# Optimization experiments

Hardware: AMD Instinct MI355X
Metric: run time of the kernel (lower is better)

## Reference

```python
import jax, jax.numpy as jnp
import numpy as np

D_MODEL = 1024
NUM_HEADS = 16
D_K = D_MODEL // NUM_HEADS
FFN_SIZE = 4096
EPS = 1e-6


def _layer_norm(x, gamma, beta):
    mu = jnp.mean(x, axis=-1, keepdims=True)
    var = jnp.var(x, axis=-1, keepdims=True)
    return (x - mu) / jnp.sqrt(var + EPS) * gamma + beta


def setup_inputs() -> dict:
    key = jax.random.key(0)
    ks = jax.random.split(key, 12)
    B, S = 2, 2048
    s_attn = 1.0 / np.sqrt(D_MODEL)
    s_ffn1 = 1.0 / np.sqrt(D_MODEL)
    s_ffn2 = 1.0 / np.sqrt(FFN_SIZE)
    return {
        "x": jax.random.normal(ks[0], (B, S, D_MODEL), dtype=jnp.float32),
        "W_q": jax.random.normal(ks[1], (D_MODEL, D_MODEL), dtype=jnp.float32) * s_attn,
        "W_k": jax.random.normal(ks[2], (D_MODEL, D_MODEL), dtype=jnp.float32) * s_attn,
        "W_v": jax.random.normal(ks[3], (D_MODEL, D_MODEL), dtype=jnp.float32) * s_attn,
        "W_o": jax.random.normal(ks[4], (D_MODEL, D_MODEL), dtype=jnp.float32) * s_attn,
        "b_o": jnp.zeros((D_MODEL,), dtype=jnp.float32),
        "W1": jax.random.normal(ks[5], (D_MODEL, FFN_SIZE), dtype=jnp.float32) * s_ffn1,
        "b1": jnp.zeros((FFN_SIZE,), dtype=jnp.float32),
        "W2": jax.random.normal(ks[6], (FFN_SIZE, D_MODEL), dtype=jnp.float32) * s_ffn2,
        "b2": jnp.zeros((D_MODEL,), dtype=jnp.float32),
        "ln1_g": jnp.ones((D_MODEL,), dtype=jnp.float32),
        "ln1_b": jnp.zeros((D_MODEL,), dtype=jnp.float32),
        "ln2_g": jnp.ones((D_MODEL,), dtype=jnp.float32),
        "ln2_b": jnp.zeros((D_MODEL,), dtype=jnp.float32),
    }


def reference(x, W_q, W_k, W_v, W_o, b_o, W1, b1, W2, b2,
              ln1_g, ln1_b, ln2_g, ln2_b):
    B, S, _ = x.shape

    # --- self-attention sublayer (pre-norm residual) ---
    h = _layer_norm(x, ln1_g, ln1_b)
    q = (h @ W_q).reshape(B, S, NUM_HEADS, D_K).transpose(0, 2, 1, 3)  # [B,H,S,Dk]
    k = (h @ W_k).reshape(B, S, NUM_HEADS, D_K).transpose(0, 2, 1, 3)
    v = (h @ W_v).reshape(B, S, NUM_HEADS, D_K).transpose(0, 2, 1, 3)
    scores = jnp.einsum("bhqd,bhkd->bhqk", q, k) / jnp.sqrt(jnp.float32(D_K))
    attn = jax.nn.softmax(scores, axis=-1)
    ctx = jnp.einsum("bhqk,bhkd->bhqd", attn, v)
    ctx = ctx.transpose(0, 2, 1, 3).reshape(B, S, D_MODEL)
    x = x + (ctx @ W_o + b_o)

    # --- FFN sublayer (pre-norm residual) ---
    h2 = _layer_norm(x, ln2_g, ln2_b)
    f = jax.nn.relu(h2 @ W1 + b1) @ W2 + b2
    return x + f
```

## Files before the change

### kernel.cpp

```cpp
#include <hip/hip_runtime.h>
#include <cstdint>
#include <cstddef>


typedef __attribute__((ext_vector_type(8))) __bf16 bf16x8;
typedef __attribute__((ext_vector_type(4))) __bf16 bf16x4;
typedef __attribute__((ext_vector_type(4))) float f32x4;

__device__ __forceinline__ void async16(const void* g, void* l) {
  __builtin_amdgcn_global_load_lds(
      (__attribute__((address_space(1))) void*)g,
      (__attribute__((address_space(3))) void*)l, 16, 0, 0);
}

__device__ __forceinline__ f32x4 mfma16(bf16x8 a, bf16x8 b, f32x4 c) {
  return __builtin_amdgcn_mfma_f32_16x16x32_bf16(a, b, c, 0, 0, 0);
}

template <int N>
__device__ __forceinline__ void wait_vmcnt() {
  if constexpr (N == 0) {
    asm volatile("s_waitcnt vmcnt(0)" ::: "memory");
  } else if constexpr (N == 3) {
    asm volatile("s_waitcnt vmcnt(3)" ::: "memory");
  } else {
    asm volatile("s_waitcnt vmcnt(4)" ::: "memory");
  }
}
__device__ __forceinline__ void barrier_raw() {
  asm volatile("s_barrier" ::: "memory");
}

__global__ __launch_bounds__(256) void transpose_all(
    const float* __restrict__ Wq, const float* __restrict__ Wk,
    const float* __restrict__ Wv, const float* __restrict__ Wo,
    const float* __restrict__ W1, const float* __restrict__ W2,
    __bf16* __restrict__ WqkvT, __bf16* __restrict__ WoT,
    __bf16* __restrict__ W1T, __bf16* __restrict__ W2T) {
  const int id = blockIdx.x;
  const float* in;
  __bf16* out;
  int ld_in, ld_out, c0, r0;
  if (id < 1024) {
    const int which = id >> 8, tl = id & 255;
    c0 = (tl & 15) * 64;
    r0 = (tl >> 4) * 64;
    ld_in = 1024;
    ld_out = 1024;
    if (which == 0) { in = Wq; out = WqkvT; }
    else if (which == 1) { in = Wk; out = WqkvT + 1048576; }
    else if (which == 2) { in = Wv; out = WqkvT + 2097152; }
    else { in = Wo; out = WoT; }
  } else if (id < 2048) {
    const int tl = id - 1024;
    c0 = (tl & 63) * 64;
    r0 = (tl >> 6) * 64;
    in = W1; out = W1T; ld_in = 4096; ld_out = 1024;
  } else {
    const int tl = id - 2048;
    c0 = (tl & 15) * 64;
    r0 = (tl >> 4) * 64;
    in = W2; out = W2T; ld_in = 1024; ld_out = 4096;
  }
  __shared__ __bf16 tile[64][65];
  const int tx = threadIdx.x & 63, ty = threadIdx.x >> 6;
#pragma unroll
  for (int i = 0; i < 16; i++) {
    int r = ty + i * 4;
    tile[r][tx] = (__bf16)in[(size_t)(r0 + r) * ld_in + c0 + tx];
  }
  __syncthreads();
#pragma unroll
  for (int i = 0; i < 16; i++) {
    int r = ty + i * 4;
    out[(size_t)(c0 + r) * ld_out + r0 + tx] = tile[tx][r];
  }
}

__global__ __launch_bounds__(256) void transpose_bf16(
    const unsigned short* __restrict__ in, unsigned short* __restrict__ out,
    int ld_in, int ld_out) {
  __shared__ unsigned short tile[64][65];
  const int c0 = blockIdx.x * 64, r0 = blockIdx.y * 64;
  const int tx = threadIdx.x & 63, ty = threadIdx.x >> 6;
#pragma unroll
  for (int i = 0; i < 16; i++) {
    int r = ty + i * 4;
    tile[r][tx] = in[(size_t)(r0 + r) * ld_in + c0 + tx];
  }
  __syncthreads();
#pragma unroll
  for (int i = 0; i < 16; i++) {
    int r = ty + i * 4;
    out[(size_t)(c0 + r) * ld_out + r0 + tx] = tile[tx][r];
  }
}

__global__ __launch_bounds__(256) void ln_kernel(
    const float* __restrict__ xin, const float* __restrict__ g,
    const float* __restrict__ bt, __bf16* __restrict__ out) {
  const int tok = blockIdx.x * 4 + (threadIdx.x >> 6);
  const int lane = threadIdx.x & 63;
  const int base0 = lane * 8, base1 = 512 + lane * 8;
  const float* xr = xin + (size_t)tok * 1024;
  float v[16];
  float4 a0 = *(const float4*)(xr + base0);
  float4 a1 = *(const float4*)(xr + base0 + 4);
  float4 a2 = *(const float4*)(xr + base1);
  float4 a3 = *(const float4*)(xr + base1 + 4);
  v[0] = a0.x; v[1] = a0.y; v[2] = a0.z; v[3] = a0.w;
  v[4] = a1.x; v[5] = a1.y; v[6] = a1.z; v[7] = a1.w;
  v[8] = a2.x; v[9] = a2.y; v[10] = a2.z; v[11] = a2.w;
  v[12] = a3.x; v[13] = a3.y; v[14] = a3.z; v[15] = a3.w;
  float s = 0.f, s2 = 0.f;
#pragma unroll
  for (int i = 0; i < 16; i++) { s += v[i]; s2 += v[i] * v[i]; }
#pragma unroll
  for (int m = 1; m < 64; m <<= 1) {
    s += __shfl_xor(s, m);
    s2 += __shfl_xor(s2, m);
  }
  const float mean = s * (1.f / 1024.f);
  const float var = s2 * (1.f / 1024.f) - mean * mean;
  const float rstd = rsqrtf(var + 1e-6f);
  float4 g0 = *(const float4*)(g + base0), g1 = *(const float4*)(g + base0 + 4);
  float4 g2 = *(const float4*)(g + base1), g3 = *(const float4*)(g + base1 + 4);
  float4 b0 = *(const float4*)(bt + base0), b1v = *(const float4*)(bt + base0 + 4);
  float4 b2v = *(const float4*)(bt + base1), b3 = *(const float4*)(bt + base1 + 4);
  float gg[16] = {g0.x, g0.y, g0.z, g0.w, g1.x, g1.y, g1.z, g1.w,
                  g2.x, g2.y, g2.z, g2.w, g3.x, g3.y, g3.z, g3.w};
  float bb[16] = {b0.x, b0.y, b0.z, b0.w, b1v.x, b1v.y, b1v.z, b1v.w,
                  b2v.x, b2v.y, b2v.z, b2v.w, b3.x, b3.y, b3.z, b3.w};
  bf16x8 o0, o1;
#pragma unroll
  for (int j = 0; j < 8; j++) {
    o0[j] = (__bf16)((v[j] - mean) * rstd * gg[j] + bb[j]);
    o1[j] = (__bf16)((v[8 + j] - mean) * rstd * gg[8 + j] + bb[8 + j]);
  }
  __bf16* op = out + (size_t)tok * 1024;
  *(bf16x8*)(op + base0) = o0;
  *(bf16x8*)(op + base1) = o1;
}

template <int EPI, int TM, int SPLITS = 1>
__global__ __launch_bounds__(256) void gemm_bt(
    const __bf16* __restrict__ A, int lda, const __bf16* __restrict__ BT,
    int ldb, void* __restrict__ C, int ldc, int Kb,
    const float* __restrict__ bias, const float* __restrict__ res, int ldres) {
  const int t = threadIdx.x;
  const int m0 = blockIdx.x * TM, n0 = blockIdx.y * 128;
  const int kz = (SPLITS > 1) ? blockIdx.z : 0;
  __shared__ __align__(16) __bf16 As[3][TM * 32];
  __shared__ __align__(16) __bf16 Bs[3][128 * 32];
  const int lane = t & 63, w = t >> 6;
  const int quad = lane >> 4, l15 = lane & 15;
  const int wm = w >> 1, wn = w & 1;
  constexpr int MF = TM / 32;
  constexpr int LOADS = TM / 64 + 2;

  f32x4 acc[MF][4] = {};

  const int swc = ((t & 3) ^ ((t >> 3) & 3)) * 8;
  const __bf16* ga = A + (size_t)(m0 + (t >> 2)) * lda + swc + (size_t)kz * Kb;
  const __bf16* gb = BT + (size_t)(n0 + (t >> 2)) * ldb + swc + (size_t)kz * Kb;
  const size_t a64 = (size_t)64 * lda, b64 = (size_t)64 * ldb;

  auto stage = [&](int buf) {
#pragma unroll
    for (int i = 0; i < TM / 64; i++)
      async16(ga + i * a64, As[buf] + t * 8 + i * 2048);
    async16(gb, Bs[buf] + t * 8);
    async16(gb + b64, Bs[buf] + t * 8 + 2048);
    ga += 32;
    gb += 32;
  };
  const int ce = (quad ^ ((l15 >> 1) & 3)) * 8;
  auto compute = [&](int buf) {
    bf16x8 af[MF], bfr[4];
#pragma unroll
    for (int i = 0; i < MF; i++)
      af[i] = *(const bf16x8*)&As[buf][(wm * (TM / 2) + i * 16 + l15) * 32 + ce];
#pragma unroll
    for (int i = 0; i < 4; i++)
      bfr[i] = *(const bf16x8*)&Bs[buf][(wn * 64 + i * 16 + l15) * 32 + ce];
#pragma unroll
    for (int mi = 0; mi < MF; mi++)
#pragma unroll
      for (int ni = 0; ni < 4; ni++)
        acc[mi][ni] = mfma16(af[mi], bfr[ni], acc[mi][ni]);
  };

  const int iters = Kb / 32;
  stage(0);
  stage(1);
  int cur = 0, stg = 2;
  for (int it = 0; it < iters - 1; ++it) {
    wait_vmcnt<LOADS>();
    barrier_raw();
    if (it + 2 < iters) stage(stg);
    compute(cur);
    cur = (cur == 2) ? 0 : cur + 1;
    stg = (stg == 2) ? 0 : stg + 1;
  }
  wait_vmcnt<0>();
  barrier_raw();
  compute(cur);

  float biasv[4];
  if constexpr (EPI != 0) {
#pragma unroll
    for (int ni = 0; ni < 4; ni++)
      biasv[ni] = bias[n0 + wn * 64 + ni * 16 + l15];
  }
  __bf16* Cb = (__bf16*)C;
  if constexpr (SPLITS > 1)
    Cb += (size_t)kz * gridDim.x * TM * ldc;
#pragma unroll
  for (int mi = 0; mi < MF; mi++)
#pragma unroll
    for (int ni = 0; ni < 4; ni++)
#pragma unroll
      for (int r = 0; r < 4; r++) {
        const int row = m0 + wm * (TM / 2) + mi * 16 + quad * 4 + r;
        const int col = n0 + wn * 64 + ni * 16 + l15;
        float v = acc[mi][ni][r];
        if constexpr (EPI == 0) {
          Cb[(size_t)row * ldc + col] = (__bf16)v;
        } else if constexpr (EPI == 1) {
          v += biasv[ni] + res[(size_t)row * ldres + col];
          ((float*)C)[(size_t)row * ldc + col] = v;
        } else {
          v += biasv[ni];
          ((__bf16*)C)[(size_t)row * ldc + col] = (__bf16)fmaxf(v, 0.f);
        }
      }
}

__global__ __launch_bounds__(256) void reduce_split(
    const __bf16* __restrict__ P, const float* __restrict__ bias,
    const float* __restrict__ res, float* __restrict__ out) {
  const int row = blockIdx.x, c = threadIdx.x * 4;
  const size_t i = (size_t)row * 1024 + c;
  bf16x4 p0 = *(const bf16x4*)(P + i);
  bf16x4 p1 = *(const bf16x4*)(P + 4194304 + i);
  float4 r = *(const float4*)(res + i);
  float4 bv = *(const float4*)(bias + c);
  float4 o;
  o.x = (float)p0[0] + (float)p1[0] + r.x + bv.x;
  o.y = (float)p0[1] + (float)p1[1] + r.y + bv.y;
  o.z = (float)p0[2] + (float)p1[2] + r.z + bv.z;
  o.w = (float)p0[3] + (float)p1[3] + r.w + bv.w;
  *(float4*)(out + i) = o;
}

__global__ __launch_bounds__(256, 4) void attn_kernel(
    const __bf16* __restrict__ QKV, const __bf16* __restrict__ VT,
    __bf16* __restrict__ ctx) {
  const int qt = blockIdx.x, bh = blockIdx.y;
  const int b = bh >> 4, h = bh & 15;
  const int t = threadIdx.x, w = t >> 6, lane = t & 63;
  const int quad = lane >> 4, l15 = lane & 15;
  const int tok0 = b * 2048;
  const int q0w = tok0 + qt * 64 + w * 16;

  __shared__ __align__(16) __bf16 Ks[128 * 64];
  __shared__ __align__(16) __bf16 VTs[64 * 128];

  const float qs = 0.18033688011112042f;
  bf16x8 qf[2];
#pragma unroll
  for (int kb = 0; kb < 2; kb++) {
    const __bf16* src =
        QKV + (size_t)(q0w + l15) * 3072 + h * 64 + kb * 32 + quad * 8;
    bf16x8 r = *(const bf16x8*)src;
#pragma unroll
    for (int j = 0; j < 8; j++) r[j] = (__bf16)((float)r[j] * qs);
    qf[kb] = r;
  }

  f32x4 lacc = {};
  f32x4 O[4] = {};

  const int krow = t >> 3;
  const int kcg = (((t & 7) ^ (krow & 7)) * 8);
  const int vrow = t >> 4;
  const int vcg = (((2 * (t & 15)) ^ ((vrow & 7) * 2)) * 4);
  const int sub = 4 * (quad & 1);
  const int qh = quad >> 1;

  for (int kt = 0; kt < 16; ++kt) {
    const int ktok = tok0 + kt * 128;
#pragma unroll
    for (int j = 0; j < 4; j++) {
      const __bf16* gp =
          QKV + (size_t)(ktok + krow + j * 32) * 3072 + 1024 + h * 64 + kcg;
      async16(gp, Ks + t * 8 + j * 2048);
    }
#pragma unroll
    for (int j = 0; j < 4; j++) {
      const __bf16* gp =
          VT + (size_t)(h * 64 + vrow + j * 16) * 4096 + ktok + vcg;
      async16(gp, VTs + t * 8 + j * 2048);
    }
    __syncthreads();

    f32x4 sT[8];
#pragma unroll
    for (int kt8 = 0; kt8 < 8; kt8++) {
      f32x4 a = {};
#pragma unroll
      for (int kb = 0; kb < 2; kb++) {
        bf16x8 kf = *(const bf16x8*)&Ks[(kt8 * 16 + l15) * 64 +
                                        (((kb * 4 + quad) ^ (l15 & 7)) * 8)];
        a = mfma16(kf, qf[kb], a);
      }
      sT[kt8] = a;
    }

    bf16x8 pf[4];
#pragma unroll
    for (int kb = 0; kb < 4; kb++)
#pragma unroll
      for (int hf = 0; hf < 2; hf++)
#pragma unroll
        for (int r = 0; r < 4; r++) {
          const float p = __builtin_amdgcn_exp2f(sT[2 * kb + hf][r]);
          lacc[r] += p;
          pf[kb][hf * 4 + r] = (__bf16)p;
        }

#pragma unroll
    for (int kb = 0; kb < 4; kb++) {
      const int g0 = (((4 * kb + qh) ^ (l15 & 7)) * 8) + sub;
      const int g1 = (((4 * kb + 2 + qh) ^ (l15 & 7)) * 8) + sub;
#pragma unroll
      for (int nd = 0; nd < 4; nd++) {
        const int base = (nd * 16 + l15) * 128;
        bf16x4 a0 = *(const bf16x4*)&VTs[base + g0];
        bf16x4 a1 = *(const bf16x4*)&VTs[base + g1];
        bf16x8 vf;
        vf[0] = a0[0]; vf[1] = a0[1]; vf[2] = a0[2]; vf[3] = a0[3];
        vf[4] = a1[0]; vf[5] = a1[1]; vf[6] = a1[2]; vf[7] = a1[3];
        O[nd] = mfma16(pf[kb], vf, O[nd]);
      }
    }
    __syncthreads();
  }

  float lsum = lacc[0] + lacc[1] + lacc[2] + lacc[3];
  lsum += __shfl_xor(lsum, 16);
  lsum += __shfl_xor(lsum, 32);
  float rl[4];
#pragma unroll
  for (int r = 0; r < 4; r++) rl[r] = 1.0f / __shfl(lsum, quad * 4 + r);
#pragma unroll
  for (int nd = 0; nd < 4; nd++)
#pragma unroll
    for (int r = 0; r < 4; r++) {
      const int tokq = q0w + quad * 4 + r;
      const int col = h * 64 + nd * 16 + l15;
      ctx[(size_t)tokq * 1024 + col] = (__bf16)(O[nd][r] * rl[r]);
    }
}

extern "C" void kernel_launch(void* const* d_in, const int* in_sizes, int n_in,
                              void* d_out, int out_size, void* d_ws,
                              size_t ws_size, hipStream_t stream) {
  (void)in_sizes; (void)n_in; (void)out_size; (void)ws_size;

  const float* x = (const float*)d_in[0];
  const float* Wq = (const float*)d_in[1];
  const float* Wk = (const float*)d_in[2];
  const float* Wv = (const float*)d_in[3];
  const float* Wo = (const float*)d_in[4];
  const float* b_o = (const float*)d_in[5];
  const float* W1 = (const float*)d_in[6];
  const float* b1 = (const float*)d_in[7];
  const float* W2 = (const float*)d_in[8];
  const float* b2 = (const float*)d_in[9];
  const float* ln1g = (const float*)d_in[10];
  const float* ln1b = (const float*)d_in[11];
  const float* ln2g = (const float*)d_in[12];
  const float* ln2b = (const float*)d_in[13];

  char* ws = (char*)d_ws;
  __bf16* WqkvT = (__bf16*)(ws + 0);
  __bf16* WoT = (__bf16*)(ws + 6291456);
  __bf16* W1T = (__bf16*)(ws + 8388608);
  __bf16* W2T = (__bf16*)(ws + 16777216);
  __bf16* h = (__bf16*)(ws + 25165824);
  __bf16* QKV = (__bf16*)(ws + 33554432);
  __bf16* VT = (__bf16*)(ws + 58720256);
  __bf16* ctx = (__bf16*)(ws + 67108864);
  float* x1 = (float*)(ws + 75497472);
  __bf16* f1 = QKV;
  __bf16* Pw2 = (__bf16*)(ws + 0);

  const dim3 blk(256);

  transpose_all<<<dim3(3072), blk, 0, stream>>>(Wq, Wk, Wv, Wo, W1, W2, WqkvT,
                                                WoT, W1T, W2T);

  ln_kernel<<<dim3(1024), blk, 0, stream>>>(x, ln1g, ln1b, h);

  gemm_bt<0, 128><<<dim3(32, 24), blk, 0, stream>>>(
      h, 1024, WqkvT, 1024, (void*)QKV, 3072, 1024, nullptr, nullptr, 0);

  transpose_bf16<<<dim3(16, 64), blk, 0, stream>>>(
      (const unsigned short*)(QKV + 2048), (unsigned short*)VT, 3072, 4096);

  attn_kernel<<<dim3(32, 32), blk, 0, stream>>>(QKV, VT, ctx);

  gemm_bt<1, 64><<<dim3(64, 8), blk, 0, stream>>>(
      ctx, 1024, WoT, 1024, (void*)x1, 1024, 1024, b_o, x, 1024);

  ln_kernel<<<dim3(1024), blk, 0, stream>>>(x1, ln2g, ln2b, h);

  gemm_bt<2, 128><<<dim3(32, 32), blk, 0, stream>>>(
      h, 1024, W1T, 1024, (void*)f1, 4096, 1024, b1, nullptr, 0);

  gemm_bt<0, 128, 2><<<dim3(32, 8, 2), blk, 0, stream>>>(
      f1, 4096, W2T, 4096, (void*)Pw2, 1024, 2048, nullptr, nullptr, 0);
  reduce_split<<<dim3(4096), blk, 0, stream>>>(Pw2, b2, x1, (float*)d_out);
}
```

Before: 347.0 us.

## Double-buffer K/V tiles and process two query sub-tiles per wave in attention

The attention kernel now stages the next K/VT tile into a second LDS buffer while computing on the current one, replacing the load-then-sync pattern. Each wave also handles 32 queries (two 16-row sub-tiles), so every K and V fragment read from LDS feeds two MFMAs, and the grid is halved to 16x32 blocks. This aims to hide global-load latency and halve K/V traffic per query, at the cost of doubled LDS (64KB), more registers, lower occupancy (launch bounds 2) and only 512 blocks.

```diff
diff --git a/kernel.cpp b/kernel.cpp
--- a/kernel.cpp
+++ b/kernel.cpp
@@ -253,7 +253,7 @@
   *(float4*)(out + i) = o;
 }
 
-__global__ __launch_bounds__(256, 4) void attn_kernel(
+__global__ __launch_bounds__(256, 2) void attn_kernel(
     const __bf16* __restrict__ QKV, const __bf16* __restrict__ VT,
     __bf16* __restrict__ ctx) {
   const int qt = blockIdx.x, bh = blockIdx.y;
@@ -261,25 +261,27 @@
   const int t = threadIdx.x, w = t >> 6, lane = t & 63;
   const int quad = lane >> 4, l15 = lane & 15;
   const int tok0 = b * 2048;
-  const int q0w = tok0 + qt * 64 + w * 16;
-
-  __shared__ __align__(16) __bf16 Ks[128 * 64];
-  __shared__ __align__(16) __bf16 VTs[64 * 128];
+  const int q0w = tok0 + qt * 128 + w * 32;
+
+  __shared__ __align__(16) __bf16 Ks[2][128 * 64];
+  __shared__ __align__(16) __bf16 VTs[2][64 * 128];
 
   const float qs = 0.18033688011112042f;
-  bf16x8 qf[2];
-#pragma unroll
-  for (int kb = 0; kb < 2; kb++) {
-    const __bf16* src =
-        QKV + (size_t)(q0w + l15) * 3072 + h * 64 + kb * 32 + quad * 8;
-    bf16x8 r = *(const bf16x8*)src;
-#pragma unroll
-    for (int j = 0; j < 8; j++) r[j] = (__bf16)((float)r[j] * qs);
-    qf[kb] = r;
-  }
-
-  f32x4 lacc = {};
-  f32x4 O[4] = {};
+  bf16x8 qf[2][2];
+#pragma unroll
+  for (int mi = 0; mi < 2; mi++)
+#pragma unroll
+    for (int kb = 0; kb < 2; kb++) {
+      const __bf16* src = QKV + (size_t)(q0w + mi * 16 + l15) * 3072 + h * 64 +
+                          kb * 32 + quad * 8;
+      bf16x8 r = *(const bf16x8*)src;
+#pragma unroll
+      for (int j = 0; j < 8; j++) r[j] = (__bf16)((float)r[j] * qs);
+      qf[mi][kb] = r;
+    }
+
+  f32x4 lacc[2] = {};
+  f32x4 O[2][4] = {};
 
   const int krow = t >> 3;
   const int kcg = (((t & 7) ^ (krow & 7)) * 8);
@@ -288,46 +290,58 @@
   const int sub = 4 * (quad & 1);
   const int qh = quad >> 1;
 
-  for (int kt = 0; kt < 16; ++kt) {
+  auto stage = [&](int buf, int kt) {
     const int ktok = tok0 + kt * 128;
 #pragma unroll
     for (int j = 0; j < 4; j++) {
       const __bf16* gp =
           QKV + (size_t)(ktok + krow + j * 32) * 3072 + 1024 + h * 64 + kcg;
-      async16(gp, Ks + t * 8 + j * 2048);
+      async16(gp, Ks[buf] + t * 8 + j * 2048);
     }
 #pragma unroll
     for (int j = 0; j < 4; j++) {
       const __bf16* gp =
           VT + (size_t)(h * 64 + vrow + j * 16) * 4096 + ktok + vcg;
-      async16(gp, VTs + t * 8 + j * 2048);
+      async16(gp, VTs[buf] + t * 8 + j * 2048);
     }
-    __syncthreads();
-
-    f32x4 sT[8];
+  };
+
+  stage(0, 0);
+  wait_vmcnt<0>();
+  barrier_raw();
+
+  int buf = 0;
+  for (int kt = 0; kt < 16; ++kt) {
+    if (kt + 1 < 16) stage(buf ^ 1, kt + 1);
+
+    f32x4 sT[2][8];
 #pragma unroll
     for (int kt8 = 0; kt8 < 8; kt8++) {
-      f32x4 a = {};
+      f32x4 a0 = {}, a1 = {};
 #pragma unroll
       for (int kb = 0; kb < 2; kb++) {
-        bf16x8 kf = *(const bf16x8*)&Ks[(kt8 * 16 + l15) * 64 +
-                                        (((kb * 4 + quad) ^ (l15 & 7)) * 8)];
-        a = mfma16(kf, qf[kb], a);
+        bf16x8 kf = *(const bf16x8*)&Ks[buf][(kt8 * 16 + l15) * 64 +
+                                            (((kb * 4 + quad) ^ (l15 & 7)) * 8)];
+        a0 = mfma16(kf, qf[0][kb], a0);
+        a1 = mfma16(kf, qf[1][kb], a1);
       }
-      sT[kt8] = a;
+      sT[0][kt8] = a0;
+      sT[1][kt8] = a1;
     }
 
-    bf16x8 pf[4];
-#pragma unroll
-    for (int kb = 0; kb < 4; kb++)
-#pragma unroll
-      for (int hf = 0; hf < 2; hf++)
-#pragma unroll
-        for (int r = 0; r < 4; r++) {
-          const float p = __builtin_amdgcn_exp2f(sT[2 * kb + hf][r]);
-          lacc[r] += p;
-          pf[kb][hf * 4 + r] = (__bf16)p;
-        }
+    bf16x8 pf[2][4];
+#pragma unroll
+    for (int mi = 0; mi < 2; mi++)
+#pragma unroll
+      for (int kb = 0; kb < 4; kb++)
+#pragma unroll
+        for (int hf = 0; hf < 2; hf++)
+#pragma unroll
+          for (int r = 0; r < 4; r++) {
+            const float p = __builtin_amdgcn_exp2f(sT[mi][2 * kb + hf][r]);
+            lacc[mi][r] += p;
+            pf[mi][kb][hf * 4 + r] = (__bf16)p;
+          }
 
 #pragma unroll
     for (int kb = 0; kb < 4; kb++) {
@@ -336,31 +350,38 @@
 #pragma unroll
       for (int nd = 0; nd < 4; nd++) {
         const int base = (nd * 16 + l15) * 128;
-        bf16x4 a0 = *(const bf16x4*)&VTs[base + g0];
-        bf16x4 a1 = *(const bf16x4*)&VTs[base + g1];
+        bf16x4 a0 = *(const bf16x4*)&VTs[buf][base + g0];
+        bf16x4 a1 = *(const bf16x4*)&VTs[buf][base + g1];
         bf16x8 vf;
         vf[0] = a0[0]; vf[1] = a0[1]; vf[2] = a0[2]; vf[3] = a0[3];
         vf[4] = a1[0]; vf[5] = a1[1]; vf[6] = a1[2]; vf[7] = a1[3];
-        O[nd] = mfma16(pf[kb], vf, O[nd]);
+        O[0][nd] = mfma16(pf[0][kb], vf, O[0][nd]);
+        O[1][nd] = mfma16(pf[1][kb], vf, O[1][nd]);
       }
     }
-    __syncthreads();
-  }
-
-  float lsum = lacc[0] + lacc[1] + lacc[2] + lacc[3];
-  lsum += __shfl_xor(lsum, 16);
-  lsum += __shfl_xor(lsum, 32);
-  float rl[4];
-#pragma unroll
-  for (int r = 0; r < 4; r++) rl[r] = 1.0f / __shfl(lsum, quad * 4 + r);
-#pragma unroll
-  for (int nd = 0; nd < 4; nd++)
-#pragma unroll
-    for (int r = 0; r < 4; r++) {
-      const int tokq = q0w + quad * 4 + r;
-      const int col = h * 64 + nd * 16 + l15;
-      ctx[(size_t)tokq * 1024 + col] = (__bf16)(O[nd][r] * rl[r]);
-    }
+
+    wait_vmcnt<0>();
+    barrier_raw();
+    buf ^= 1;
+  }
+
+#pragma unroll
+  for (int mi = 0; mi < 2; mi++) {
+    float lsum = lacc[mi][0] + lacc[mi][1] + lacc[mi][2] + lacc[mi][3];
+    lsum += __shfl_xor(lsum, 16);
+    lsum += __shfl_xor(lsum, 32);
+    float rl[4];
+#pragma unroll
+    for (int r = 0; r < 4; r++) rl[r] = 1.0f / __shfl(lsum, quad * 4 + r);
+#pragma unroll
+    for (int nd = 0; nd < 4; nd++)
+#pragma unroll
+      for (int r = 0; r < 4; r++) {
+        const int tokq = q0w + mi * 16 + quad * 4 + r;
+        const int col = h * 64 + nd * 16 + l15;
+        ctx[(size_t)tokq * 1024 + col] = (__bf16)(O[mi][nd][r] * rl[r]);
+      }
+  }
 }
 
 extern "C" void kernel_launch(void* const* d_in, const int* in_sizes, int n_in,
@@ -409,7 +430,7 @@
   transpose_bf16<<<dim3(16, 64), blk, 0, stream>>>(
       (const unsigned short*)(QKV + 2048), (unsigned short*)VT, 3072, 4096);
 
-  attn_kernel<<<dim3(32, 32), blk, 0, stream>>>(QKV, VT, ctx);
+  attn_kernel<<<dim3(16, 32), blk, 0, stream>>>(QKV, VT, ctx);
 
   gemm_bt<1, 64><<<dim3(64, 8), blk, 0, stream>>>(
       ctx, 1024, WoT, 1024, (void*)x1, 1024, 1024, b_o, x, 1024);
```

New measurement: 339.6 us. 1.02x faster.
